# Kernel tuning notes

Hardware: AMD Instinct MI355X
Metric: run time of the kernel (lower is better)

Reference implementation:

```python
import math
import jax, jax.numpy as jnp
import numpy as np

L, H, D, DFF = 4, 8, 1024, 4096
RGB, AUD = 1024, 128
D_ATT, D_HOP, NCLS = 128, 4, 3862
B, T = 32, 300
EPS = 1e-6


def setup_inputs() -> dict:
    key = jax.random.key(0)
    ks = iter(jax.random.split(key, 40))
    s = 0.02
    p = {
        'padded_frame_rgbs': jax.random.uniform(next(ks), (B, T, RGB), jnp.float32),
        'padded_frame_audios': jax.random.uniform(next(ks), (B, T, AUD), jnp.float32),
        'embed_W': jax.random.normal(next(ks), (RGB + AUD, D), jnp.float32) * s,
        'embed_b': jnp.zeros((D,), jnp.float32),
        'Wq': jax.random.normal(next(ks), (L, D, D), jnp.float32) * s,
        'bq': jnp.zeros((L, D), jnp.float32),
        'Wk': jax.random.normal(next(ks), (L, D, D), jnp.float32) * s,
        'bk': jnp.zeros((L, D), jnp.float32),
        'Wv': jax.random.normal(next(ks), (L, D, D), jnp.float32) * s,
        'bv': jnp.zeros((L, D), jnp.float32),
        'Wo': jax.random.normal(next(ks), (L, D, D), jnp.float32) * s,
        'bo': jnp.zeros((L, D), jnp.float32),
        'ln1_a': jnp.ones((L, D), jnp.float32),
        'ln1_b': jnp.zeros((L, D), jnp.float32),
        'W1f': jax.random.normal(next(ks), (L, D, DFF), jnp.float32) * s,
        'b1f': jnp.zeros((L, DFF), jnp.float32),
        'W2f': jax.random.normal(next(ks), (L, DFF, D), jnp.float32) * s,
        'b2f': jnp.zeros((L, D), jnp.float32),
        'ln2_a': jnp.ones((L, D), jnp.float32),
        'ln2_b': jnp.zeros((L, D), jnp.float32),
        'fn_a': jnp.ones((D,), jnp.float32),
        'fn_b': jnp.zeros((D,), jnp.float32),
        'cw1': jax.random.normal(next(ks), (D, D_ATT), jnp.float32) * s,
        'cb1': jnp.zeros((D_ATT,), jnp.float32),
        'cw2': jax.random.normal(next(ks), (D_ATT, D_HOP), jnp.float32) * s,
        'cb2': jnp.zeros((D_HOP,), jnp.float32),
        'cw3': jax.random.normal(next(ks), (D_HOP * D, DFF), jnp.float32) * s,
        'cb3': jnp.zeros((DFF,), jnp.float32),
        'cw4': jax.random.normal(next(ks), (DFF, NCLS), jnp.float32) * s,
        'cb4': jnp.zeros((NCLS,), jnp.float32),
    }
    return p


def layernorm(x, a, b):
    # torch: a*(x-mean)/(std+eps)+b with unbiased std (ddof=1)
    mean = jnp.mean(x, axis=-1, keepdims=True)
    std = jnp.std(x, axis=-1, keepdims=True, ddof=1)
    return a * (x - mean) / (std + EPS) + b


def positional_encoding(T, D):
    pos = jnp.arange(T, dtype=jnp.float32)[:, None]
    div = jnp.exp(jnp.arange(0, D, 2, dtype=jnp.float32) * (-math.log(10000.0) / D))
    ang = pos * div  # [T, D/2]
    pe = jnp.stack([jnp.sin(ang), jnp.cos(ang)], axis=-1).reshape(T, D)
    return pe


def mha(x, Wq, bq, Wk, bk, Wv, bv, Wo, bo):
    dk = D // H
    q = (x @ Wq + bq).reshape(B, T, H, dk)
    k = (x @ Wk + bk).reshape(B, T, H, dk)
    v = (x @ Wv + bv).reshape(B, T, H, dk)
    scores = jnp.einsum('bthd,bshd->bhts', q, k) / math.sqrt(dk)
    p = jax.nn.softmax(scores, axis=-1)
    o = jnp.einsum('bhts,bshd->bthd', p, v).reshape(B, T, D)
    return o @ Wo + bo


def forward(padded_frame_rgbs, padded_frame_audios, embed_W, embed_b,
            Wq, bq, Wk, bk, Wv, bv, Wo, bo, ln1_a, ln1_b,
            W1f, b1f, W2f, b2f, ln2_a, ln2_b, fn_a, fn_b,
            cw1, cb1, cw2, cb2, cw3, cb3, cw4, cb4):
    feats = jnp.concatenate([padded_frame_rgbs / 255.0,
                             padded_frame_audios / 255.0], axis=2)
    x = (feats @ embed_W + embed_b) * math.sqrt(D)
    x = x + positional_encoding(T, D)[None]
    for i in range(L):
        x = x + mha(layernorm(x, ln1_a[i], ln1_b[i]),
                    Wq[i], bq[i], Wk[i], bk[i], Wv[i], bv[i], Wo[i], bo[i])
        h = layernorm(x, ln2_a[i], ln2_b[i])
        x = x + (jax.nn.relu(h @ W1f[i] + b1f[i]) @ W2f[i] + b2f[i])
    x = layernorm(x, fn_a, fn_b)
    # embedded classifier (multi-hop attention pooling)
    alpha = jnp.tanh(x @ cw1 + cb1) @ cw2 + cb2            # [B, T, D_HOP]
    alpha = jax.nn.softmax(alpha.transpose(0, 2, 1), -1)   # [B, D_HOP, T]
    ws = jnp.einsum('bht,btd->bhd', alpha, x).reshape(B, D_HOP * D)
    out = jnp.tanh(ws @ cw3 + cb3) @ cw4 + cb4             # [B, NCLS]
    return out, alpha


def reference(padded_frame_rgbs, padded_frame_audios, embed_W, embed_b,
              Wq, bq, Wk, bk, Wv, bv, Wo, bo, ln1_a, ln1_b,
              W1f, b1f, W2f, b2f, ln2_a, ln2_b, fn_a, fn_b,
              cw1, cb1, cw2, cb2, cw3, cb3, cw4, cb4):
    return forward(padded_frame_rgbs, padded_frame_audios, embed_W, embed_b,
                   Wq, bq, Wk, bk, Wv, bv, Wo, bo, ln1_a, ln1_b,
                   W1f, b1f, W2f, b2f, ln2_a, ln2_b, fn_a, fn_b,
                   cw1, cb1, cw2, cb2, cw3, cb3, cw4, cb4)
```

## Files before the change

### kernel.cpp

```cpp
#include <hip/hip_runtime.h>
#include <stdint.h>

#define NTOK 9600
#define TT   300
#define DD   1024
#define HH   8
#define DFF  4096
#define FIN  1152
#define DATT 128
#define NCLS 3862
#define TP   320
#define NQT  19

typedef unsigned short u16;
typedef __attribute__((ext_vector_type(8))) short short8;
typedef __attribute__((ext_vector_type(4))) float f32x4;

__device__ __forceinline__ int imin(int a, int b){ return a < b ? a : b; }

__device__ __forceinline__ u16 f2bf(float f){
    union { float f; uint32_t u; } v; v.f = f;
    uint32_t u = v.u;
    return (u16)((u + 0x7fffu + ((u >> 16) & 1u)) >> 16);
}
// ... 74 lines not shown
        const float* __restrict__ bk, const float* __restrict__ bv, float* __restrict__ out)
{
    const int i = blockIdx.x * 256 + threadIdx.x;
    if (i >= 4 * 3072) return;
    const int l = i / 3072, c = i % 3072;
    float v;
    if      (c < 1024) v = bq[l * 1024 + c];
    else if (c < 2048) v = bk[l * 1024 + c - 1024];
    else               v = bv[l * 1024 + c - 2048];
    out[i] = v;
}

template<int WF>
__global__ void __launch_bounds__(256) ln_kernel(const float* __restrict__ xin,
        const float* __restrict__ ga, const float* __restrict__ gb,
        u16* __restrict__ ob, float* of)
{
    const int row = blockIdx.x, t = threadIdx.x;
    const float4 xv = *(const float4*)(xin + (size_t)row * 1024 + t * 4);
    float s1 = xv.x + xv.y + xv.z + xv.w;
    float s2 = xv.x * xv.x + xv.y * xv.y + xv.z * xv.z + xv.w * xv.w;
    #pragma unroll
    for (int o = 1; o < 64; o <<= 1) { s1 += __shfl_xor(s1, o); s2 += __shfl_xor(s2, o); }
    __shared__ float r1[4], r2[4];
    const int lane = t & 63, wid = t >> 6;
    if (lane == 0) { r1[wid] = s1; r2[wid] = s2; }
    __syncthreads();
    s1 = r1[0] + r1[1] + r1[2] + r1[3];
    s2 = r2[0] + r2[1] + r2[2] + r2[3];
    const float mean = s1 * (1.0f / 1024.0f);
    const float var  = (s2 - 1024.0f * mean * mean) * (1.0f / 1023.0f);
    const float inv  = 1.0f / (sqrtf(fmaxf(var, 0.f)) + 1e-6f);
    const float4 av  = *(const float4*)(ga + t * 4);
    const float4 bv  = *(const float4*)(gb + t * 4);
    const float y0 = av.x * (xv.x - mean) * inv + bv.x;
    const float y1 = av.y * (xv.y - mean) * inv + bv.y;
    const float y2 = av.z * (xv.z - mean) * inv + bv.z;
    const float y3 = av.w * (xv.w - mean) * inv + bv.w;
    ushort4 o4; o4.x = f2bf(y0); o4.y = f2bf(y1); o4.z = f2bf(y2); o4.w = f2bf(y3);
    *(ushort4*)(ob + (size_t)row * 1024 + t * 4) = o4;
    if (WF) {
        float4 yo; yo.x = y0; yo.y = y1; yo.z = y2; yo.w = y3;
        *(float4*)(of + (size_t)row * 1024 + t * 4) = yo;
    }
}

#define EPI_EMBED        0
#define EPI_QKV          1
#define EPI_B_RELU_BF16  2
#define EPI_B_RES_F32    3
#define EPI_B_TANH_F32   4
#define EPI_ACC_F32      5
#define EPI_PART         6

template<int EPI, int SWZ>
__global__ void __launch_bounds__(256) gemm_k(const u16* __restrict__ A, const u16* __restrict__ Bt,
        const float* __restrict__ bias, const float* extra,
        float* outF, u16* outB, u16* outB2, u16* outB3, int M, int N, int K,
        int lda, int ldb, int kchunk)
{
    __shared__ __align__(16) u16 As[2][4096];
    __shared__ __align__(16) u16 Bs[2][4096];
    const int tid = threadIdx.x;
    int bm, bn;
    if (SWZ) {
        int lin = blockIdx.y * gridDim.x + blockIdx.x;
        const int nwg = gridDim.x * gridDim.y;
        const int cpx = nwg >> 3;
        lin = (lin & 7) * cpx + (lin >> 3);
        bm = lin / gridDim.x;
        bn = lin - bm * gridDim.x;
    } else {
        bm = blockIdx.y; bn = blockIdx.x;
    }
    const int lane = tid & 63, wid = tid >> 6;
    const int lg = lane >> 4, lr = lane & 15;
    const int wr = wid >> 1, wc = wid & 1;

    int koff = 0, Keff = K;
    if (kchunk > 0) { koff = blockIdx.z * kchunk; Keff = kchunk; }

    const int srow = tid >> 2;
    const int skc  = (tid & 3) * 8;
    const u16* ap0 = A  + (size_t)imin(bm * 128 + srow,      M - 1) * lda + skc + koff;
    const u16* ap1 = A  + (size_t)imin(bm * 128 + srow + 64, M - 1) * lda + skc + koff;
    const u16* bp0 = Bt + (size_t)imin(bn * 128 + srow,      N - 1) * ldb + skc + koff;
    const u16* bp1 = Bt + (size_t)imin(bn * 128 + srow + 64, N - 1) * ldb + skc + koff;

    f32x4 acc[4][4] = {};

    auto STAGE = [&](int b, int k0) {
        gll16(ap0 + k0, &As[b][tid * 8]);
        gll16(ap1 + k0, &As[b][2048 + tid * 8]);
        gll16(bp0 + k0, &Bs[b][tid * 8]);
        gll16(bp1 + k0, &Bs[b][2048 + tid * 8]);
    };
    auto COMPUTE = [&](int b) {
        short8 af[4], bf[4];
        #pragma unroll
        for (int m = 0; m < 4; ++m)
            af[m] = *(const short8*)(&As[b][(wr * 64 + m * 16 + lr) * 32 + lg * 8]);
        #pragma unroll
        for (int n = 0; n < 4; ++n)
            bf[n] = *(const short8*)(&Bs[b][(wc * 64 + n * 16 + lr) * 32 + lg * 8]);
        #pragma unroll
        for (int m = 0; m < 4; ++m)
            #pragma unroll
            for (int n = 0; n < 4; ++n)
                acc[m][n] = mfma16(af[m], bf[n], acc[m][n]);
    };

    STAGE(0, 0);
    __syncthreads();
    int cur = 0;
    for (int k0 = 32; k0 < Keff; k0 += 32) {
        STAGE(cur ^ 1, k0);
        COMPUTE(cur);
        __syncthreads();
        cur ^= 1;
    }
    COMPUTE(cur);

    #pragma unroll
    for (int m = 0; m < 4; ++m) {
        const int rb = bm * 128 + wr * 64 + m * 16 + lg * 4;
        #pragma unroll
        for (int n = 0; n < 4; ++n) {
            const int col = bn * 128 + wc * 64 + n * 16 + lr;
            if (col >= N) continue;
            const float bvl = (EPI == EPI_PART || EPI == EPI_ACC_F32) ? 0.f : bias[col];
            #pragma unroll
            for (int j = 0; j < 4; ++j) {
                const int r = rb + j;
                if (r >= M) continue;
                const float v = acc[m][n][j];
                const size_t oi = (size_t)r * N + col;
                if      (EPI == EPI_EMBED)       outF[oi] = (v + bvl) * 32.0f + extra[(size_t)(r % 300) * 1024 + col];
                else if (EPI == EPI_QKV) {
                    const int q = col >> 10, lc = col & 1023;
                    u16* dst = (q == 0) ? outB : ((q == 1) ? outB2 : outB3);
                    dst[(size_t)r * 1024 + lc] = f2bf(v + bvl);
                }
                else if (EPI == EPI_B_RELU_BF16) outB[oi] = f2bf(fmaxf(v + bvl, 0.f));
                else if (EPI == EPI_B_RES_F32)   outF[oi] = v + bvl + extra[oi];
                else if (EPI == EPI_B_TANH_F32)  outF[oi] = tanhf(v + bvl);
                else if (EPI == EPI_ACC_F32)     outF[oi] = v + extra[oi];
                else if (EPI == EPI_PART)        outF[(size_t)blockIdx.z * M * N + oi] = v;
            }
        }
    }
}

template<int EPI>
__global__ void __launch_bounds__(512, 2) gemm_big(const u16* __restrict__ A, const u16* __restrict__ Bt,
        const float* __restrict__ bias, const float* __restrict__ extra,
        float* outF, u16* outB, u16* outB2, u16* outB3,
        int M, int N, int K, int lda, int ldb, int kchunk)
{
    __shared__ __align__(16) u16 LA[2][256 * 32];
    __shared__ __align__(16) u16 LB[2][256 * 32];
    const int tid = threadIdx.x;
    int lin = blockIdx.x;
    const int nwg = gridDim.x;
    if ((nwg & 7) == 0) { const int cpx = nwg >> 3; lin = (lin & 7) * cpx + (lin >> 3); }
    int z = 0;
    if (kchunk > 0) { z = lin & 1; lin >>= 1; }
    const int ntN = N >> 8;
    const int bm = lin / ntN, bn = lin - (lin / ntN) * ntN;
    const int koff = z * kchunk;
    const int Keff = (kchunk > 0) ? kchunk : K;

    const int lane = tid & 63, wid = tid >> 6;
    const int wm = wid >> 2, wn = wid & 3;
    const int lg = lane >> 4, lr = lane & 15;

    const int prow = tid >> 2;
    const int skg  = (((tid & 3) ^ ((tid >> 3) & 3)) * 8);
    const u16* asrc0 = A  + (size_t)imin(bm * 256 + prow,       M - 1) * lda + skg + koff;
    const u16* asrc1 = A  + (size_t)imin(bm * 256 + prow + 128, M - 1) * lda + skg + koff;
    const u16* bsrc0 = Bt + (size_t)(bn * 256 + prow)       * ldb + skg + koff;
    const u16* bsrc1 = Bt + (size_t)(bn * 256 + prow + 128) * ldb + skg + koff;

    auto STAGE = [&](int s, int k0) {
        gll16(asrc0 + k0, &LA[s][tid * 8]);
        gll16(asrc1 + k0, &LA[s][4096 + tid * 8]);
        gll16(bsrc0 + k0, &LB[s][tid * 8]);
        gll16(bsrc1 + k0, &LB[s][4096 + tid * 8]);
    };

    const int kge = (lg ^ ((lr >> 1) & 3)) * 8;
    int aoff[8], boff[4];
    #pragma unroll
    for (int m = 0; m < 8; ++m) aoff[m] = (wm * 128 + m * 16 + lr) * 32 + kge;
    #pragma unroll
    for (int n = 0; n < 4; ++n) boff[n] = (wn * 64 + n * 16 + lr) * 32 + kge;

    f32x4 acc[8][4] = {};
    short8 af[8], bf[4];

    const int nk = Keff >> 5;
    STAGE(0, 0);
    STAGE(1, 32);
    asm volatile("s_waitcnt vmcnt(4)" ::: "memory");
    asm volatile("s_barrier" ::: "memory");
    __builtin_amdgcn_sched_barrier(0);

    auto BODY = [&](int t, int s, bool doStage) {
        #pragma unroll
        for (int m = 0; m < 8; ++m) af[m] = *(const short8*)(&LA[s][aoff[m]]);
        #pragma unroll
        for (int n = 0; n < 4; ++n) bf[n] = *(const short8*)(&LB[s][boff[n]]);
        asm volatile("s_waitcnt lgkmcnt(0)" ::: "memory");
        __builtin_amdgcn_sched_barrier(0);
        __builtin_amdgcn_s_setprio(1);
        #pragma unroll
        for (int m = 0; m < 4; ++m)
            #pragma unroll
            for (int n = 0; n < 4; ++n)
                acc[m][n] = mfma16(af[m], bf[n], acc[m][n]);
        __builtin_amdgcn_s_setprio(0);
        asm volatile("s_barrier" ::: "memory");
        __builtin_amdgcn_sched_barrier(0);
        if (doStage) STAGE(s, (t + 2) * 32);
        __builtin_amdgcn_s_setprio(1);
        #pragma unroll
        for (int m = 4; m < 8; ++m)
            #pragma unroll
            for (int n = 0; n < 4; ++n)
                acc[m][n] = mfma16(af[m], bf[n], acc[m][n]);
        __builtin_amdgcn_s_setprio(0);
    };

    for (int t = 0; t < nk - 2; ++t) {
        BODY(t, t & 1, true);
        asm volatile("s_waitcnt vmcnt(4)" ::: "memory");
        __builtin_amdgcn_sched_barrier(0);
        asm volatile("s_barrier" ::: "memory");
        __builtin_amdgcn_sched_barrier(0);
    }
    BODY(nk - 2, (nk - 2) & 1, false);
    asm volatile("s_waitcnt vmcnt(0)" ::: "memory");
    __builtin_amdgcn_sched_barrier(0);
    asm volatile("s_barrier" ::: "memory");
    __builtin_amdgcn_sched_barrier(0);
    BODY(nk - 1, (nk - 1) & 1, false);

    #pragma unroll
    for (int m = 0; m < 8; ++m) {
        const int rb = bm * 256 + wm * 128 + m * 16 + lg * 4;
        #pragma unroll
        for (int n = 0; n < 4; ++n) {
            const int col = bn * 256 + wn * 64 + n * 16 + lr;
            const float bvl = (EPI == EPI_PART) ? 0.f : bias[col];
            #pragma unroll
            for (int j = 0; j < 4; ++j) {
                const int r = rb + j;
                if (r >= M) continue;
                const float v = acc[m][n][j] + bvl;
                const size_t oi = (size_t)r * N + col;
                if (EPI == EPI_QKV) {
                    const int q = col >> 10, lc = col & 1023;
                    u16* dst = (q == 0) ? outB : ((q == 1) ? outB2 : outB3);
                    dst[(size_t)r * 1024 + lc] = f2bf(v);
                }
                else if (EPI == EPI_B_RELU_BF16) outB[oi] = f2bf(fmaxf(v, 0.f));
                else if (EPI == EPI_B_RES_F32)   outF[oi] = v + extra[oi];
                else if (EPI == EPI_EMBED)       outF[oi] = v * 32.0f + extra[(size_t)(r % 300) * 1024 + col];
                else if (EPI == EPI_PART)        outF[(size_t)z * M * N + oi] = v;
            }
        }
    }
}

template<int EPI>
__global__ void __launch_bounds__(256, 3) gemm_mid(const u16* __restrict__ A, const u16* __restrict__ Bt,
        const float* __restrict__ bias, const float* __restrict__ extra,
        float* outF, u16* outB, u16* outB2, u16* outB3,
        int M, int N, int K, int lda, int ldb)
{
    __shared__ __align__(16) u16 LA[2][128 * 32];
    __shared__ __align__(16) u16 LB[2][128 * 32];
    const int tid = threadIdx.x;
    int lin = blockIdx.x;
    const int nwg = gridDim.x;
    if ((nwg & 7) == 0) { const int cpx = nwg >> 3; lin = (lin & 7) * cpx + (lin >> 3); }
    const int ntN = N >> 7;
    const int bm = lin / ntN, bn = lin - (lin / ntN) * ntN;

    const int lane = tid & 63, wid = tid >> 6;
    const int wr = wid >> 1, wc = wid & 1;
    const int lg = lane >> 4, lr = lane & 15;

    const int prow = tid >> 2;
    const int skg  = (((tid & 3) ^ ((tid >> 3) & 3)) * 8);
    const u16* asrc0 = A  + (size_t)imin(bm * 128 + prow,      M - 1) * lda + skg;
    const u16* asrc1 = A  + (size_t)imin(bm * 128 + prow + 64, M - 1) * lda + skg;
    const u16* bsrc0 = Bt + (size_t)(bn * 128 + prow)      * ldb + skg;
    const u16* bsrc1 = Bt + (size_t)(bn * 128 + prow + 64) * ldb + skg;

    auto STAGE = [&](int s, int k0) {
        gll16(asrc0 + k0, &LA[s][tid * 8]);
        gll16(asrc1 + k0, &LA[s][2048 + tid * 8]);
        gll16(bsrc0 + k0, &LB[s][tid * 8]);
        gll16(bsrc1 + k0, &LB[s][2048 + tid * 8]);
    };

    const int kge = (lg ^ ((lr >> 1) & 3)) * 8;
    int aoff[4], boff[4];
    #pragma unroll
    for (int m = 0; m < 4; ++m) aoff[m] = (wr * 64 + m * 16 + lr) * 32 + kge;
    #pragma unroll
    for (int n = 0; n < 4; ++n) boff[n] = (wc * 64 + n * 16 + lr) * 32 + kge;

    f32x4 acc[4][4] = {};
    short8 af[4], bf[4];

    const int nk = K >> 5;
    STAGE(0, 0);
    STAGE(1, 32);
    asm volatile("s_waitcnt vmcnt(4)" ::: "memory");
    asm volatile("s_barrier" ::: "memory");
    __builtin_amdgcn_sched_barrier(0);

    auto BODY = [&](int t, int s, bool doStage) {
        #pragma unroll
        for (int m = 0; m < 4; ++m) af[m] = *(const short8*)(&LA[s][aoff[m]]);
        #pragma unroll
        for (int n = 0; n < 4; ++n) bf[n] = *(const short8*)(&LB[s][boff[n]]);
        __builtin_amdgcn_s_setprio(1);
        #pragma unroll
        for (int m = 0; m < 2; ++m)
            #pragma unroll
            for (int n = 0; n < 4; ++n)
                acc[m][n] = mfma16(af[m], bf[n], acc[m][n]);
        __builtin_amdgcn_s_setprio(0);
        asm volatile("s_waitcnt lgkmcnt(0)" ::: "memory");
        __builtin_amdgcn_sched_barrier(0);
        asm volatile("s_barrier" ::: "memory");
        __builtin_amdgcn_sched_barrier(0);
        if (doStage) STAGE(s, (t + 2) * 32);
        __builtin_amdgcn_s_setprio(1);
        #pragma unroll
        for (int m = 2; m < 4; ++m)
            #pragma unroll
            for (int n = 0; n < 4; ++n)
                acc[m][n] = mfma16(af[m], bf[n], acc[m][n]);
        __builtin_amdgcn_s_setprio(0);
    };

    for (int t = 0; t < nk - 2; ++t) {
        BODY(t, t & 1, true);
        asm volatile("s_waitcnt vmcnt(4)" ::: "memory");
        __builtin_amdgcn_sched_barrier(0);
        asm volatile("s_barrier" ::: "memory");
        __builtin_amdgcn_sched_barrier(0);
    }
    BODY(nk - 2, (nk - 2) & 1, false);
    asm volatile("s_waitcnt vmcnt(0)" ::: "memory");
    __builtin_amdgcn_sched_barrier(0);
    asm volatile("s_barrier" ::: "memory");
    __builtin_amdgcn_sched_barrier(0);
    BODY(nk - 1, (nk - 1) & 1, false);

    #pragma unroll
    for (int m = 0; m < 4; ++m) {
        const int rb = bm * 128 + wr * 64 + m * 16 + lg * 4;
        #pragma unroll
        for (int n = 0; n < 4; ++n) {
            const int col = bn * 128 + wc * 64 + n * 16 + lr;
            const float bvl = bias[col];
            #pragma unroll
            for (int j = 0; j < 4; ++j) {
                const int r = rb + j;
                if (r >= M) continue;
                const float v = acc[m][n][j] + bvl;
                const size_t oi = (size_t)r * N + col;
                if      (EPI == EPI_B_RES_F32)   outF[oi] = v + extra[oi];
                else if (EPI == EPI_EMBED)       outF[oi] = v * 32.0f + extra[(size_t)(r % 300) * 1024 + col];
                else if (EPI == EPI_B_RELU_BF16) outB[oi] = f2bf(fmaxf(v, 0.f));
                else if (EPI == EPI_B_TANH_F32)  outF[oi] = tanhf(v);
                else if (EPI == EPI_QKV) {
                    const int q = col >> 10, lc = col & 1023;
                    u16* dst = (q == 0) ? outB : ((q == 1) ? outB2 : outB3);
                    dst[(size_t)r * 1024 + lc] = f2bf(v);
                }
            }
        }
    }
}

template<int TANH>
__global__ void __launch_bounds__(256) redk_kernel(const float* __restrict__ part,
        const float* __restrict__ bias, float* outF, u16* outB, int M, int N, int Z)
{
    const int i = blockIdx.x * 256 + threadIdx.x;
    if (i >= M * N) return;
    const int col = i % N;
    float s = 0.f;
    for (int z = 0; z < Z; ++z) s += part[(size_t)z * M * N + i];
    s += bias[col];
    if (TANH) outB[i] = f2bf(tanhf(s));
    else      outF[i] = s;
}

__global__ void __launch_bounds__(512) attn_scores_kernel(const u16* __restrict__ Qb,
        const u16* __restrict__ Kb, u16* __restrict__ P)
{
    __shared__ __align__(16) u16 Ks[304 * 128];
    __shared__ __align__(16) u16 Ps[8][16][TP];
    const int bh = blockIdx.x, b = bh >> 3, h = bh & 7;
    const int tid = threadIdx.x, lane = tid & 63, wid = tid >> 6;
    const int lg = lane >> 4, lr = lane & 15;

    for (int c = tid; c < 304 * 16; c += 512) {
        const int kv = c >> 4, part = c & 15;
        const int tok = b * 300 + imin(kv, 299);
        const short8 v = *(const short8*)(Kb + (size_t)tok * 1024 + h * 128 + part * 8);
        int byte_ = kv * 256 + part * 16;
        byte_ ^= (kv & 7) << 4;
        *(short8*)((char*)Ks + byte_) = v;
    }
    __syncthreads();

    const float scale = 0.08838834764831845f;
    for (int qt = wid; qt < NQT; qt += 8) {
        f32x4 acc[NQT] = {};
        const int qtok = b * 300 + imin(qt * 16 + lr, 299);
        const u16* qrow = Qb + (size_t)qtok * 1024 + h * 128;
        #pragma unroll
        for (int kk = 0; kk < 4; ++kk) {
            const short8 aq = *(const short8*)(qrow + kk * 32 + lg * 8);
            #pragma unroll
            for (int nt = 0; nt < NQT; ++nt) {
                const int kvrow = nt * 16 + lr;
                int byte_ = kvrow * 256 + kk * 64 + lg * 16;
                byte_ ^= (kvrow & 7) << 4;
                const short8 bk = *(const short8*)((char*)Ks + byte_);
                acc[nt] = mfma16(aq, bk, acc[nt]);
            }
        }
        const int sw = lg << 3;
        #pragma unroll
        for (int j = 0; j < 4; ++j) {
            float vals[NQT];
            float m = -1e30f;
            #pragma unroll
            for (int nt = 0; nt < NQT; ++nt) {
                float s = acc[nt][j] * scale;
                if (nt * 16 + lr >= 300) s = -1e30f;
                vals[nt] = s;
                m = fmaxf(m, s);
            }
            #pragma unroll
            for (int o = 1; o < 16; o <<= 1) m = fmaxf(m, __shfl_xor(m, o));
            float sum = 0.f;
            #pragma unroll
            for (int nt = 0; nt < NQT; ++nt) { const float e = __expf(vals[nt] - m); vals[nt] = e; sum += e; }
            #pragma unroll
            for (int o = 1; o < 16; o <<= 1) sum += __shfl_xor(sum, o);
            const float inv = 1.0f / sum;
            const int row = lg * 4 + j;
            #pragma unroll
            for (int nt = 0; nt < NQT; ++nt) Ps[wid][row][(nt * 16 + lr) ^ sw] = f2bf(vals[nt] * inv);
            Ps[wid][row][(304 + lr) ^ sw] = 0;
        }
        asm volatile("s_waitcnt lgkmcnt(0)" ::: "memory");
        __builtin_amdgcn_sched_barrier(0);
        #pragma unroll
        for (int it = 0; it < 10; ++it) {
            const int idx = it * 64 + lane;
            const int row = idx / 40, c8 = idx - row * 40;
            const int swr = ((row >> 2) & 3) << 3;
            const short8 v8 = *(const short8*)(&Ps[wid][row][(c8 * 8) ^ swr]);
            const int q = qt * 16 + row;
            if (q < 300) *(short8*)(P + ((size_t)bh * 300 + q) * TP + c8 * 8) = v8;
        }
    }
}

__global__ void __launch_bounds__(512) attn_pv_kernel(const u16* __restrict__ P,
        const u16* __restrict__ Vb, u16* __restrict__ O)
{
    __shared__ __align__(16) u16 Vs[128 * TP];
    __shared__ __align__(16) u16 Os[8][16][128];
    const int bh = blockIdx.x, b = bh >> 3, h = bh & 7;
    const int tid = threadIdx.x, lane = tid & 63, wid = tid >> 6;
    const int lg = lane >> 4, lr = lane & 15;

    for (int c = tid; c < 304 * 16; c += 512) {
        const int kv = c >> 4, dp = c & 15;
        const int tok = b * 300 + imin(kv, 299);
        const short8 v = *(const short8*)(Vb + (size_t)tok * 1024 + h * 128 + dp * 8);
        #pragma unroll
        for (int jj = 0; jj < 8; ++jj) {
            const int d = dp * 8 + jj;
            int byte_ = d * (TP * 2) + kv * 2;
            byte_ ^= (d & 7) << 4;
            *(u16*)((char*)Vs + byte_) = (u16)v[jj];
        }
    }
    for (int c = tid; c < 128 * 16; c += 512) {
        const int d = c >> 4, kv = 304 + (c & 15);
        int byte_ = d * (TP * 2) + kv * 2;
        byte_ ^= (d & 7) << 4;
        *(u16*)((char*)Vs + byte_) = 0;
    }
    __syncthreads();

    for (int qt = wid; qt < NQT; qt += 8) {
        f32x4 acc[8] = {};
        const int q = imin(qt * 16 + lr, 299);
        const u16* prow = P + ((size_t)bh * 300 + q) * TP;
        #pragma unroll
        for (int kk = 0; kk < 10; ++kk) {
            const short8 ap = *(const short8*)(prow + kk * 32 + lg * 8);
            #pragma unroll
            for (int nt = 0; nt < 8; ++nt) {
                const int d = nt * 16 + lr;
                int byte_ = d * (TP * 2) + kk * 64 + lg * 16;
                byte_ ^= (d & 7) << 4;
                const short8 bv8 = *(const short8*)((char*)Vs + byte_);
                acc[nt] = mfma16(ap, bv8, acc[nt]);
            }
        }
        const int sw = lg << 3;
        #pragma unroll
        for (int nt = 0; nt < 8; ++nt)
            #pragma unroll
            for (int j = 0; j < 4; ++j)
                Os[wid][lg * 4 + j][(nt * 16 + lr) ^ sw] = f2bf(acc[nt][j]);
        asm volatile("s_waitcnt lgkmcnt(0)" ::: "memory");
        __builtin_amdgcn_sched_barrier(0);
        #pragma unroll
        for (int it = 0; it < 4; ++it) {
            const int idx = it * 64 + lane;
            const int row = idx >> 4, c8 = idx & 15;
            const int swr = ((row >> 2) & 3) << 3;
            const short8 v8 = *(const short8*)(&Os[wid][row][(c8 * 8) ^ swr]);
            const int qq = qt * 16 + row;
            if (qq < 300)
                *(short8*)(O + ((size_t)(b * 300 + qq)) * 1024 + h * 128 + c8 * 8) = v8;
        }
    }
}

__global__ void __launch_bounds__(256) logits_kernel(const float* __restrict__ a1,
        const float* __restrict__ cw2, const float* __restrict__ cb2, float* __restrict__ out)
{
    const int tok = blockIdx.x * 4 + (threadIdx.x >> 6);
    const int lane = threadIdx.x & 63;
    if (tok >= NTOK) return;
    const float v0 = a1[(size_t)tok * 128 + lane];
    const float v1 = a1[(size_t)tok * 128 + 64 + lane];
    #pragma unroll
    for (int hp = 0; hp < 4; ++hp) {
        float s = v0 * cw2[lane * 4 + hp] + v1 * cw2[(64 + lane) * 4 + hp];
        #pragma unroll
        for (int o = 1; o < 64; o <<= 1) s += __shfl_xor(s, o);
        if (lane == 0) out[(size_t)tok * 4 + hp] = s + cb2[hp];
    }
}

__global__ void __launch_bounds__(512) softmaxT_kernel(const float* __restrict__ lgt,
        float* __restrict__ alpha, float* __restrict__ outAlpha)
{
    const int bh = blockIdx.x;
    const int b = bh >> 2, hp = bh & 3;
    const int t = threadIdx.x;
    const float v = (t < 300) ? lgt[((size_t)(b * 300 + t)) * 4 + hp] : -1e30f;
    float m = v;
    #pragma unroll
    for (int o = 1; o < 64; o <<= 1) m = fmaxf(m, __shfl_xor(m, o));
    __shared__ float rm[8], rs[8];
    const int lane = t & 63, wid = t >> 6;
    if (lane == 0) rm[wid] = m;
    __syncthreads();
    m = rm[0];
    #pragma unroll
    for (int i = 1; i < 8; ++i) m = fmaxf(m, rm[i]);
    const float e = (t < 300) ? __expf(v - m) : 0.f;
    float s = e;
    #pragma unroll
    for (int o = 1; o < 64; o <<= 1) s += __shfl_xor(s, o);
    if (lane == 0) rs[wid] = s;
    __syncthreads();
    s = rs[0] + rs[1] + rs[2] + rs[3] + rs[4] + rs[5] + rs[6] + rs[7];
    if (t < 300) {
        const float a = e / s;
        alpha[(size_t)bh * 300 + t] = a;
        outAlpha[(size_t)bh * 300 + t] = a;
    }
}

__global__ void __launch_bounds__(256) pool_kernel(const float* __restrict__ alpha,
        const float* __restrict__ xln, float* __restrict__ wsp)
{
    const int bh = blockIdx.x, b = bh >> 2;
    const int d = blockIdx.y * 256 + threadIdx.x;
    const float* xp = xln + (size_t)b * 300 * 1024 + d;
    const float* al = alpha + (size_t)bh * 300;
    float acc = 0.f;
    for (int t = 0; t < 300; ++t) acc += al[t] * xp[(size_t)t * 1024];
    wsp[(size_t)bh * 1024 + d] = acc;
}

extern "C" void kernel_launch(void* const* d_in, const int* in_sizes, int n_in,
                              void* d_out, int out_size, void* d_ws, size_t ws_size,
                              hipStream_t stream)
{
    const float* rgb     = (const float*)d_in[0];
    const float* aud     = (const float*)d_in[1];
    const float* embed_W = (const float*)d_in[2];
    const float* embed_b = (const float*)d_in[3];
    const float* Wq      = (const float*)d_in[4];
    const float* bq      = (const float*)d_in[5];
    const float* Wk      = (const float*)d_in[6];
    const float* bk      = (const float*)d_in[7];
    const float* Wv      = (const float*)d_in[8];
    const float* bv      = (const float*)d_in[9];
    const float* Wo      = (const float*)d_in[10];
    const float* bo      = (const float*)d_in[11];
    const float* ln1_a   = (const float*)d_in[12];
    const float* ln1_b   = (const float*)d_in[13];
    const float* W1f     = (const float*)d_in[14];
    const float* b1f     = (const float*)d_in[15];
    const float* W2f     = (const float*)d_in[16];
    const float* b2f     = (const float*)d_in[17];
    const float* ln2_a   = (const float*)d_in[18];
    const float* ln2_b   = (const float*)d_in[19];
    const float* fn_a    = (const float*)d_in[20];
    const float* fn_b    = (const float*)d_in[21];
    const float* cw1     = (const float*)d_in[22];
    const float* cb1     = (const float*)d_in[23];
    const float* cw2     = (const float*)d_in[24];
    const float* cb2     = (const float*)d_in[25];
    const float* cw3     = (const float*)d_in[26];
    const float* cb3     = (const float*)d_in[27];
    const float* cw4     = (const float*)d_in[28];
    const float* cb4     = (const float*)d_in[29];

    const bool bigS = ws_size >= ((size_t)238 << 20);
    const size_t Ssz = bigS ? (size_t)NTOK * DFF * 2 : (size_t)256 * 300 * TP * 2;

    char* base = (char*)d_ws;
    size_t off = 0;
    auto alloc = [&](size_t bytes) -> char* {
        char* p = base + off; off += (bytes + 255) & ~(size_t)255; return p; };

    float* x    = (float*)alloc((size_t)NTOK * DD * 4);
    float* pe   = (float*)alloc((size_t)TT * DD * 4);
    u16*  hbuf  = (u16*) alloc((size_t)NTOK * DD * 2);
    u16*  Qb    = (u16*) alloc((size_t)NTOK * DD * 2);
    u16*  Kb    = (u16*) alloc((size_t)NTOK * DD * 2);
    u16*  Vb    = (u16*) alloc((size_t)NTOK * DD * 2);
    u16*  S     = (u16*) alloc(Ssz);
    float* lgts = (float*)alloc((size_t)NTOK * 4 * 4);
    float* alph = (float*)alloc((size_t)128 * 300 * 4);
    float* wsp  = (float*)alloc((size_t)32 * 4096 * 4);
    u16*  wsb   = (u16*) alloc((size_t)32 * 4096 * 2);
    u16*  t3b   = (u16*) alloc((size_t)32 * 4096 * 2);
    float* bqkv = (float*)alloc((size_t)4 * 3072 * 4);
    u16*  eWt   = (u16*) alloc((size_t)1024 * 1152 * 2);
    u16*  WqkvT = (u16*) alloc((size_t)3 * 1024 * 1024 * 2);
    u16*  WoT   = (u16*) alloc((size_t)1024 * 1024 * 2);
    u16*  W1T   = (u16*) alloc((size_t)DFF * DD * 2);
    u16*  W2T   = (u16*) alloc((size_t)DD * DFF * 2);
    u16*  c1T   = (u16*) alloc((size_t)128 * 1024 * 2);
    if (off > ws_size) return;

    u16*  featsb = S;
    u16*  pbuf   = S;
    u16*  midc   = S;
    u16*  Ob     = hbuf;
    float* xln   = (float*)Qb;
    u16*  xlnb   = Vb;
    float* a1    = (float*)S;
    u16*  c3T    = (u16*)x;
    u16*  c4T    = S;
    float* part  = (float*)hbuf;
    float* outv     = (float*)d_out;
    float* outAlpha = outv + (size_t)32 * NCLS;

    const dim3 blk(256);

    pe_kernel<<<(TT * DD + 255) / 256, blk, 0, stream>>>(pe);
    feats_kernel<<<(int)(((size_t)NTOK * FIN + 255) / 256), blk, 0, stream>>>(rgb, aud, featsb);
    qkvbias_kernel<<<(4 * 3072 + 255) / 256, blk, 0, stream>>>(bq, bk, bv, bqkv);

    auto wconv = [&](const float* W, u16* Wt, int K, int N) {
        dim3 g((N + 31) / 32, (K + 31) / 32);
        wconv_kernel<<<g, dim3(32, 8), 0, stream>>>(W, Wt, K, N);
    };
    wconv(embed_W, eWt, FIN, DD);
    wconv(cw1, c1T, DD, DATT);

    gemm_mid<EPI_EMBED><<<600, blk, 0, stream>>>(featsb, eWt, embed_b, pe, x,
            nullptr, nullptr, nullptr, NTOK, DD, FIN, FIN, FIN);

    for (int i = 0; i < 4; ++i) {
        wconv3_kernel<<<dim3(32, 32, 3), dim3(32, 8), 0, stream>>>(
                Wq + (size_t)i * DD * DD, Wk + (size_t)i * DD * DD, Wv + (size_t)i * DD * DD, WqkvT);
        wconv(Wo  + (size_t)i * DD * DD,  WoT, DD, DD);
        wconv(W1f + (size_t)i * DD * DFF, W1T, DD, DFF);
        wconv(W2f + (size_t)i * DFF * DD, W2T, DFF, DD);

        ln_kernel<0><<<NTOK, blk, 0, stream>>>(x, ln1_a + (size_t)i * DD, ln1_b + (size_t)i * DD, hbuf, nullptr);
        gemm_mid<EPI_QKV><<<1800, blk, 0, stream>>>(hbuf, WqkvT, bqkv + (size_t)i * 3072, nullptr,
                nullptr, Qb, Kb, Vb, NTOK, 3072, DD, DD, DD);
        attn_scores_kernel<<<256, dim3(512), 0, stream>>>(Qb, Kb, pbuf);
        attn_pv_kernel<<<256, dim3(512), 0, stream>>>(pbuf, Vb, Ob);
        gemm_mid<EPI_B_RES_F32><<<600, blk, 0, stream>>>(Ob, WoT, bo + (size_t)i * DD, x, x,
                nullptr, nullptr, nullptr, NTOK, DD, DD, DD, DD);
        ln_kernel<0><<<NTOK, blk, 0, stream>>>(x, ln2_a + (size_t)i * DD, ln2_b + (size_t)i * DD, hbuf, nullptr);
        if (bigS) {
            gemm_mid<EPI_B_RELU_BF16><<<2400, blk, 0, stream>>>(hbuf, W1T, b1f + (size_t)i * DFF,
                    nullptr, nullptr, midc, nullptr, nullptr, NTOK, DFF, DD, DD, DD);
            gemm_mid<EPI_B_RES_F32><<<600, blk, 0, stream>>>(midc, W2T, b2f + (size_t)i * DD, x, x,
                    nullptr, nullptr, nullptr, NTOK, DD, DFF, DFF, DFF);
        } else {
            for (int h = 0; h < 2; ++h) {
                gemm_big<EPI_B_RELU_BF16><<<304, dim3(512), 0, stream>>>(hbuf, W1T + (size_t)h * 2048 * DD,
                        b1f + (size_t)i * DFF + h * 2048, nullptr, nullptr, midc, nullptr, nullptr,
                        NTOK, 2048, DD, DD, DD, 0);
                if (h == 0)
                    gemm_k<EPI_B_RES_F32, 1><<<dim3(8, 75), blk, 0, stream>>>(midc, W2T + (size_t)h * 2048,
                            b2f + (size_t)i * DD, x, x, nullptr, nullptr, nullptr, NTOK, DD, 2048, 2048, DFF, 0);
                else
                    gemm_k<EPI_ACC_F32, 1><<<dim3(8, 75), blk, 0, stream>>>(midc, W2T + (size_t)h * 2048,
                            b2f + (size_t)i * DD, x, x, nullptr, nullptr, nullptr, NTOK, DD, 2048, 2048, DFF, 0);
            }
        }
    }

    ln_kernel<1><<<NTOK, blk, 0, stream>>>(x, fn_a, fn_b, xlnb, xln);
    wconv(cw3, c3T, 4096, DFF);
    gemm_mid<EPI_B_TANH_F32><<<75, blk, 0, stream>>>(xlnb, c1T, cb1, nullptr, a1,
            nullptr, nullptr, nullptr, NTOK, DATT, DD, DD, DD);
    logits_kernel<<<2400, blk, 0, stream>>>(a1, cw2, cb2, lgts);
    wconv(cw4, c4T, DFF, NCLS);
    softmaxT_kernel<<<128, dim3(512), 0, stream>>>(lgts, alph, outAlpha);
    pool_kernel<<<dim3(128, 4), blk, 0, stream>>>(alph, xln, wsp);
    f2bf_kernel<<<(32 * 4096 + 255) / 256, blk, 0, stream>>>(wsp, wsb, 32 * 4096);

    gemm_k<EPI_PART, 0><<<dim3(32, 1, 8), blk, 0, stream>>>(wsb, c3T, nullptr, nullptr, part,
            nullptr, nullptr, nullptr, 32, 4096, 4096, 4096, 4096, 512);
    redk_kernel<1><<<(32 * 4096 + 255) / 256, blk, 0, stream>>>(part, cb3, nullptr, t3b, 32, 4096, 8);
    gemm_k<EPI_PART, 0><<<dim3(31, 1, 8), blk, 0, stream>>>(t3b, c4T, nullptr, nullptr, part,
            nullptr, nullptr, nullptr, 32, NCLS, 4096, 4096, 4096, 512);
    redk_kernel<0><<<(32 * NCLS + 255) / 256, blk, 0, stream>>>(part, cb4, outv, nullptr, 32, NCLS, 8);
}
```

Before: 2.079 ms.

## Split attention kernels across two blocks per head to double grid size

The attention score kernel now launches two blocks per (batch, head), each handling half of the query tiles, and writes softmax probabilities directly to global memory instead of staging through shared memory. The PV kernel splits the 128-wide head dimension into two 64-wide halves per block, halving its shared V tile and output staging. Both get launch_bounds occupancy hints and a 512-block grid to fill more compute units than the previous 256 blocks. The costs are that the score kernel reloads the full K tile in each half-block, and its direct stores are scattered 2-byte writes rather than coalesced 16-byte ones. With 10 query tiles per half and 8 waves, some waves also do two iterations while others idle.

Measured after the change: 2.808 ms. 35.0% more time.

```diff
diff --git a/kernel.cpp b/kernel.cpp
--- a/kernel.cpp
+++ b/kernel.cpp
@@ -501,12 +501,12 @@
     else      outF[i] = s;
 }
 
-__global__ void __launch_bounds__(512) attn_scores_kernel(const u16* __restrict__ Qb,
+__global__ void __launch_bounds__(512, 4) attn_scores_kernel(const u16* __restrict__ Qb,
         const u16* __restrict__ Kb, u16* __restrict__ P)
 {
     __shared__ __align__(16) u16 Ks[304 * 128];
-    __shared__ __align__(16) u16 Ps[8][16][TP];
-    const int bh = blockIdx.x, b = bh >> 3, h = bh & 7;
+    const int bh = blockIdx.x >> 1, half = blockIdx.x & 1;
+    const int b = bh >> 3, h = bh & 7;
     const int tid = threadIdx.x, lane = tid & 63, wid = tid >> 6;
     const int lg = lane >> 4, lr = lane & 15;
 
@@ -521,7 +521,8 @@
     __syncthreads();
 
     const float scale = 0.08838834764831845f;
-    for (int qt = wid; qt < NQT; qt += 8) {
+    const int qtEnd = imin(NQT, half * 10 + 10);
+    for (int qt = half * 10 + wid; qt < qtEnd; qt += 8) {
         f32x4 acc[NQT] = {};
         const int qtok = b * 300 + imin(qt * 16 + lr, 299);
         const u16* qrow = Qb + (size_t)qtok * 1024 + h * 128;
@@ -537,7 +538,6 @@
                 acc[nt] = mfma16(aq, bk, acc[nt]);
             }
         }
-        const int sw = lg << 3;
         #pragma unroll
         for (int j = 0; j < 4; ++j) {
             float vals[NQT];
@@ -557,38 +557,31 @@
             #pragma unroll
             for (int o = 1; o < 16; o <<= 1) sum += __shfl_xor(sum, o);
             const float inv = 1.0f / sum;
-            const int row = lg * 4 + j;
-            #pragma unroll
-            for (int nt = 0; nt < NQT; ++nt) Ps[wid][row][(nt * 16 + lr) ^ sw] = f2bf(vals[nt] * inv);
-            Ps[wid][row][(304 + lr) ^ sw] = 0;
+            const int q = qt * 16 + lg * 4 + j;
+            if (q < 300) {
+                u16* prow = P + ((size_t)bh * 300 + q) * TP;
+                #pragma unroll
+                for (int nt = 0; nt < NQT; ++nt) prow[nt * 16 + lr] = f2bf(vals[nt] * inv);
+                prow[304 + lr] = 0;
+            }
         }
-        asm volatile("s_waitcnt lgkmcnt(0)" ::: "memory");
-        __builtin_amdgcn_sched_barrier(0);
-        #pragma unroll
-        for (int it = 0; it < 10; ++it) {
-            const int idx = it * 64 + lane;
-            const int row = idx / 40, c8 = idx - row * 40;
-            const int swr = ((row >> 2) & 3) << 3;
-            const short8 v8 = *(const short8*)(&Ps[wid][row][(c8 * 8) ^ swr]);
-            const int q = qt * 16 + row;
-            if (q < 300) *(short8*)(P + ((size_t)bh * 300 + q) * TP + c8 * 8) = v8;
-        }
-    }
-}
-
-__global__ void __launch_bounds__(512) attn_pv_kernel(const u16* __restrict__ P,
+    }
+}
+
+__global__ void __launch_bounds__(512, 4) attn_pv_kernel(const u16* __restrict__ P,
         const u16* __restrict__ Vb, u16* __restrict__ O)
 {
-    __shared__ __align__(16) u16 Vs[128 * TP];
-    __shared__ __align__(16) u16 Os[8][16][128];
-    const int bh = blockIdx.x, b = bh >> 3, h = bh & 7;
+    __shared__ __align__(16) u16 Vs[64 * TP];
+    __shared__ __align__(16) u16 Os[8][16][64];
+    const int bh = blockIdx.x >> 1, dh = blockIdx.x & 1;
+    const int b = bh >> 3, h = bh & 7;
     const int tid = threadIdx.x, lane = tid & 63, wid = tid >> 6;
     const int lg = lane >> 4, lr = lane & 15;
 
-    for (int c = tid; c < 304 * 16; c += 512) {
-        const int kv = c >> 4, dp = c & 15;
+    for (int c = tid; c < 304 * 8; c += 512) {
+        const int kv = c >> 3, dp = c & 7;
         const int tok = b * 300 + imin(kv, 299);
-        const short8 v = *(const short8*)(Vb + (size_t)tok * 1024 + h * 128 + dp * 8);
+        const short8 v = *(const short8*)(Vb + (size_t)tok * 1024 + h * 128 + dh * 64 + dp * 8);
         #pragma unroll
         for (int jj = 0; jj < 8; ++jj) {
             const int d = dp * 8 + jj;
@@ -597,7 +590,7 @@
             *(u16*)((char*)Vs + byte_) = (u16)v[jj];
         }
     }
-    for (int c = tid; c < 128 * 16; c += 512) {
+    for (int c = tid; c < 64 * 16; c += 512) {
         const int d = c >> 4, kv = 304 + (c & 15);
         int byte_ = d * (TP * 2) + kv * 2;
         byte_ ^= (d & 7) << 4;
@@ -606,14 +599,14 @@
     __syncthreads();
 
     for (int qt = wid; qt < NQT; qt += 8) {
-        f32x4 acc[8] = {};
+        f32x4 acc[4] = {};
         const int q = imin(qt * 16 + lr, 299);
         const u16* prow = P + ((size_t)bh * 300 + q) * TP;
         #pragma unroll
         for (int kk = 0; kk < 10; ++kk) {
             const short8 ap = *(const short8*)(prow + kk * 32 + lg * 8);
             #pragma unroll
-            for (int nt = 0; nt < 8; ++nt) {
+            for (int nt = 0; nt < 4; ++nt) {
                 const int d = nt * 16 + lr;
                 int byte_ = d * (TP * 2) + kk * 64 + lg * 16;
                 byte_ ^= (d & 7) << 4;
@@ -623,21 +616,21 @@
         }
         const int sw = lg << 3;
         #pragma unroll
-        for (int nt = 0; nt < 8; ++nt)
+        for (int nt = 0; nt < 4; ++nt)
             #pragma unroll
             for (int j = 0; j < 4; ++j)
                 Os[wid][lg * 4 + j][(nt * 16 + lr) ^ sw] = f2bf(acc[nt][j]);
         asm volatile("s_waitcnt lgkmcnt(0)" ::: "memory");
         __builtin_amdgcn_sched_barrier(0);
         #pragma unroll
-        for (int it = 0; it < 4; ++it) {
+        for (int it = 0; it < 2; ++it) {
             const int idx = it * 64 + lane;
-            const int row = idx >> 4, c8 = idx & 15;
+            const int row = idx >> 3, c8 = idx & 7;
             const int swr = ((row >> 2) & 3) << 3;
             const short8 v8 = *(const short8*)(&Os[wid][row][(c8 * 8) ^ swr]);
             const int qq = qt * 16 + row;
             if (qq < 300)
-                *(short8*)(O + ((size_t)(b * 300 + qq)) * 1024 + h * 128 + c8 * 8) = v8;
+                *(short8*)(O + ((size_t)(b * 300 + qq)) * 1024 + h * 128 + dh * 64 + c8 * 8) = v8;
         }
     }
 }
@@ -805,8 +798,8 @@
         ln_kernel<0><<<NTOK, blk, 0, stream>>>(x, ln1_a + (size_t)i * DD, ln1_b + (size_t)i * DD, hbuf, nullptr);
         gemm_mid<EPI_QKV><<<1800, blk, 0, stream>>>(hbuf, WqkvT, bqkv + (size_t)i * 3072, nullptr,
                 nullptr, Qb, Kb, Vb, NTOK, 3072, DD, DD, DD);
-        attn_scores_kernel<<<256, dim3(512), 0, stream>>>(Qb, Kb, pbuf);
-        attn_pv_kernel<<<256, dim3(512), 0, stream>>>(pbuf, Vb, Ob);
+        attn_scores_kernel<<<512, dim3(512), 0, stream>>>(Qb, Kb, pbuf);
+        attn_pv_kernel<<<512, dim3(512), 0, stream>>>(pbuf, Vb, Ob);
         gemm_mid<EPI_B_RES_F32><<<600, blk, 0, stream>>>(Ob, WoT, bo + (size_t)i * DD, x, x,
                 nullptr, nullptr, nullptr, NTOK, DD, DD, DD, DD);
         ln_kernel<0><<<NTOK, blk, 0, stream>>>(x, ln2_a + (size_t)i * DD, ln2_b + (size_t)i * DD, hbuf, nullptr);
```

## Add 128x128 GEMM with 64-wide K step and use it for most projections

Applied to the files above, without the earlier changes.

Adds gemm_mid64, a 128x128-tile GEMM that stages 64 K-elements per iteration with a wider XOR swizzle and splits the MFMA work into two halves so the second half's LDS reads overlap the first half's compute. It replaces gemm_mid for the embed, QKV, output projection and FFN paths, and replaces the 256x256 gemm_big for the FFN up-projection. The aim is to halve barrier and loop overhead per K and improve latency hiding. In exchange each block uses twice the LDS with occupancy lowered to 2, and the FFN1 path loses the larger tile's data reuse.

After: 2.308 ms. 11.0% more time.

```diff
diff --git a/kernel.cpp b/kernel.cpp
--- a/kernel.cpp
+++ b/kernel.cpp
@@ -250,127 +250,6 @@
 }
 
 template<int EPI>
-__global__ void __launch_bounds__(512, 2) gemm_big(const u16* __restrict__ A, const u16* __restrict__ Bt,
-        const float* __restrict__ bias, const float* __restrict__ extra,
-        float* outF, u16* outB, u16* outB2, u16* outB3,
-        int M, int N, int K, int lda, int ldb, int kchunk)
-{
-    __shared__ __align__(16) u16 LA[2][256 * 32];
-    __shared__ __align__(16) u16 LB[2][256 * 32];
-    const int tid = threadIdx.x;
-    int lin = blockIdx.x;
-    const int nwg = gridDim.x;
-    if ((nwg & 7) == 0) { const int cpx = nwg >> 3; lin = (lin & 7) * cpx + (lin >> 3); }
-    int z = 0;
-    if (kchunk > 0) { z = lin & 1; lin >>= 1; }
-    const int ntN = N >> 8;
-    const int bm = lin / ntN, bn = lin - (lin / ntN) * ntN;
-    const int koff = z * kchunk;
-    const int Keff = (kchunk > 0) ? kchunk : K;
-
-    const int lane = tid & 63, wid = tid >> 6;
-    const int wm = wid >> 2, wn = wid & 3;
-    const int lg = lane >> 4, lr = lane & 15;
-
-    const int prow = tid >> 2;
-    const int skg  = (((tid & 3) ^ ((tid >> 3) & 3)) * 8);
-    const u16* asrc0 = A  + (size_t)imin(bm * 256 + prow,       M - 1) * lda + skg + koff;
-    const u16* asrc1 = A  + (size_t)imin(bm * 256 + prow + 128, M - 1) * lda + skg + koff;
-    const u16* bsrc0 = Bt + (size_t)(bn * 256 + prow)       * ldb + skg + koff;
-    const u16* bsrc1 = Bt + (size_t)(bn * 256 + prow + 128) * ldb + skg + koff;
-
-    auto STAGE = [&](int s, int k0) {
-        gll16(asrc0 + k0, &LA[s][tid * 8]);
-        gll16(asrc1 + k0, &LA[s][4096 + tid * 8]);
-        gll16(bsrc0 + k0, &LB[s][tid * 8]);
-        gll16(bsrc1 + k0, &LB[s][4096 + tid * 8]);
-    };
-
-    const int kge = (lg ^ ((lr >> 1) & 3)) * 8;
-    int aoff[8], boff[4];
-    #pragma unroll
-    for (int m = 0; m < 8; ++m) aoff[m] = (wm * 128 + m * 16 + lr) * 32 + kge;
-    #pragma unroll
-    for (int n = 0; n < 4; ++n) boff[n] = (wn * 64 + n * 16 + lr) * 32 + kge;
-
-    f32x4 acc[8][4] = {};
-    short8 af[8], bf[4];
-
-    const int nk = Keff >> 5;
-    STAGE(0, 0);
-    STAGE(1, 32);
-    asm volatile("s_waitcnt vmcnt(4)" ::: "memory");
-    asm volatile("s_barrier" ::: "memory");
-    __builtin_amdgcn_sched_barrier(0);
-
-    auto BODY = [&](int t, int s, bool doStage) {
-        #pragma unroll
-        for (int m = 0; m < 8; ++m) af[m] = *(const short8*)(&LA[s][aoff[m]]);
-        #pragma unroll
-        for (int n = 0; n < 4; ++n) bf[n] = *(const short8*)(&LB[s][boff[n]]);
-        asm volatile("s_waitcnt lgkmcnt(0)" ::: "memory");
-        __builtin_amdgcn_sched_barrier(0);
-        __builtin_amdgcn_s_setprio(1);
-        #pragma unroll
-        for (int m = 0; m < 4; ++m)
-            #pragma unroll
-            for (int n = 0; n < 4; ++n)
-                acc[m][n] = mfma16(af[m], bf[n], acc[m][n]);
-        __builtin_amdgcn_s_setprio(0);
-        asm volatile("s_barrier" ::: "memory");
-        __builtin_amdgcn_sched_barrier(0);
-        if (doStage) STAGE(s, (t + 2) * 32);
-        __builtin_amdgcn_s_setprio(1);
-        #pragma unroll
-        for (int m = 4; m < 8; ++m)
-            #pragma unroll
-            for (int n = 0; n < 4; ++n)
-                acc[m][n] = mfma16(af[m], bf[n], acc[m][n]);
-        __builtin_amdgcn_s_setprio(0);
-    };
-
-    for (int t = 0; t < nk - 2; ++t) {
-        BODY(t, t & 1, true);
-        asm volatile("s_waitcnt vmcnt(4)" ::: "memory");
-        __builtin_amdgcn_sched_barrier(0);
-        asm volatile("s_barrier" ::: "memory");
-        __builtin_amdgcn_sched_barrier(0);
-    }
-    BODY(nk - 2, (nk - 2) & 1, false);
-    asm volatile("s_waitcnt vmcnt(0)" ::: "memory");
-    __builtin_amdgcn_sched_barrier(0);
-    asm volatile("s_barrier" ::: "memory");
-    __builtin_amdgcn_sched_barrier(0);
-    BODY(nk - 1, (nk - 1) & 1, false);
-
-    #pragma unroll
-    for (int m = 0; m < 8; ++m) {
-        const int rb = bm * 256 + wm * 128 + m * 16 + lg * 4;
-        #pragma unroll
-        for (int n = 0; n < 4; ++n) {
-            const int col = bn * 256 + wn * 64 + n * 16 + lr;
-            const float bvl = (EPI == EPI_PART) ? 0.f : bias[col];
-            #pragma unroll
-            for (int j = 0; j < 4; ++j) {
-                const int r = rb + j;
-                if (r >= M) continue;
-                const float v = acc[m][n][j] + bvl;
-                const size_t oi = (size_t)r * N + col;
-                if (EPI == EPI_QKV) {
-                    const int q = col >> 10, lc = col & 1023;
-                    u16* dst = (q == 0) ? outB : ((q == 1) ? outB2 : outB3);
-                    dst[(size_t)r * 1024 + lc] = f2bf(v);
-                }
-                else if (EPI == EPI_B_RELU_BF16) outB[oi] = f2bf(fmaxf(v, 0.f));
-                else if (EPI == EPI_B_RES_F32)   outF[oi] = v + extra[oi];
-                else if (EPI == EPI_EMBED)       outF[oi] = v * 32.0f + extra[(size_t)(r % 300) * 1024 + col];
-                else if (EPI == EPI_PART)        outF[(size_t)z * M * N + oi] = v;
-            }
-        }
-    }
-}
-
-template<int EPI>
 __global__ void __launch_bounds__(256, 3) gemm_mid(const u16* __restrict__ A, const u16* __restrict__ Bt,
         const float* __restrict__ bias, const float* __restrict__ extra,
         float* outF, u16* outB, u16* outB2, u16* outB3,
@@ -477,6 +356,133 @@
                 else if (EPI == EPI_EMBED)       outF[oi] = v * 32.0f + extra[(size_t)(r % 300) * 1024 + col];
                 else if (EPI == EPI_B_RELU_BF16) outB[oi] = f2bf(fmaxf(v, 0.f));
                 else if (EPI == EPI_B_TANH_F32)  outF[oi] = tanhf(v);
+                else if (EPI == EPI_QKV) {
+                    const int q = col >> 10, lc = col & 1023;
+                    u16* dst = (q == 0) ? outB : ((q == 1) ? outB2 : outB3);
+                    dst[(size_t)r * 1024 + lc] = f2bf(v);
+                }
+            }
+        }
+    }
+}
+
+template<int EPI>
+__global__ void __launch_bounds__(256, 2) gemm_mid64(const u16* __restrict__ A, const u16* __restrict__ Bt,
+        const float* __restrict__ bias, const float* __restrict__ extra,
+        float* outF, u16* outB, u16* outB2, u16* outB3,
+        int M, int N, int K, int lda, int ldb)
+{
+    __shared__ __align__(16) u16 LA[2][128 * 64];
+    __shared__ __align__(16) u16 LB[2][128 * 64];
+    const int tid = threadIdx.x;
+    int lin = blockIdx.x;
+    const int nwg = gridDim.x;
+    if ((nwg & 7) == 0) { const int cpx = nwg >> 3; lin = (lin & 7) * cpx + (lin >> 3); }
+    const int ntN = N >> 7;
+    const int bm = lin / ntN, bn = lin - (lin / ntN) * ntN;
+
+    const int lane = tid & 63, wid = tid >> 6;
+    const int wr = wid >> 1, wc = wid & 1;
+    const int lg = lane >> 4, lr = lane & 15;
+
+    const int prow = tid >> 3;
+    const int skg  = (((tid & 7) ^ ((tid >> 3) & 7)) * 8);
+    const u16* asrc[4];
+    const u16* bsrc[4];
+    #pragma unroll
+    for (int L = 0; L < 4; ++L) {
+        asrc[L] = A  + (size_t)imin(bm * 128 + L * 32 + prow, M - 1) * lda + skg;
+        bsrc[L] = Bt + (size_t)(bn * 128 + L * 32 + prow) * ldb + skg;
+    }
+
+    auto STAGE = [&](int s, int k0) {
+        #pragma unroll
+        for (int L = 0; L < 4; ++L) gll16(asrc[L] + k0, &LA[s][L * 2048 + tid * 8]);
+        #pragma unroll
+        for (int L = 0; L < 4; ++L) gll16(bsrc[L] + k0, &LB[s][L * 2048 + tid * 8]);
+    };
+
+    int aoff[2][4], boff[2][4];
+    #pragma unroll
+    for (int c = 0; c < 2; ++c) {
+        #pragma unroll
+        for (int m = 0; m < 4; ++m)
+            aoff[c][m] = (wr * 64 + m * 16 + lr) * 64 + ((((c << 2) + lg) ^ (lr & 7)) * 8);
+        #pragma unroll
+        for (int n = 0; n < 4; ++n)
+            boff[c][n] = (wc * 64 + n * 16 + lr) * 64 + ((((c << 2) + lg) ^ (lr & 7)) * 8);
+    }
+
+    f32x4 acc[4][4] = {};
+    short8 af0[4], bf0[4], af1[4], bf1[4];
+
+    const int nk = K >> 6;
+    STAGE(0, 0);
+    STAGE(1, 64);
+    asm volatile("s_waitcnt vmcnt(8)" ::: "memory");
+    asm volatile("s_barrier" ::: "memory");
+    __builtin_amdgcn_sched_barrier(0);
+
+    auto BODY = [&](int t, int s, bool doStage) {
+        #pragma unroll
+        for (int m = 0; m < 4; ++m) af0[m] = *(const short8*)(&LA[s][aoff[0][m]]);
+        #pragma unroll
+        for (int n = 0; n < 4; ++n) bf0[n] = *(const short8*)(&LB[s][boff[0][n]]);
+        __builtin_amdgcn_s_setprio(1);
+        #pragma unroll
+        for (int m = 0; m < 4; ++m)
+            #pragma unroll
+            for (int n = 0; n < 4; ++n)
+                acc[m][n] = mfma16(af0[m], bf0[n], acc[m][n]);
+        __builtin_amdgcn_s_setprio(0);
+        #pragma unroll
+        for (int m = 0; m < 4; ++m) af1[m] = *(const short8*)(&LA[s][aoff[1][m]]);
+        #pragma unroll
+        for (int n = 0; n < 4; ++n) bf1[n] = *(const short8*)(&LB[s][boff[1][n]]);
+        asm volatile("s_waitcnt lgkmcnt(0)" ::: "memory");
+        __builtin_amdgcn_sched_barrier(0);
+        asm volatile("s_barrier" ::: "memory");
+        __builtin_amdgcn_sched_barrier(0);
+        if (doStage) STAGE(s, (t + 2) * 64);
+        __builtin_amdgcn_s_setprio(1);
+        #pragma unroll
+        for (int m = 0; m < 4; ++m)
+            #pragma unroll
+            for (int n = 0; n < 4; ++n)
+                acc[m][n] = mfma16(af1[m], bf1[n], acc[m][n]);
+        __builtin_amdgcn_s_setprio(0);
+    };
+
+    for (int t = 0; t < nk - 2; ++t) {
+        BODY(t, t & 1, true);
+        asm volatile("s_waitcnt vmcnt(8)" ::: "memory");
+        __builtin_amdgcn_sched_barrier(0);
+        asm volatile("s_barrier" ::: "memory");
+        __builtin_amdgcn_sched_barrier(0);
+    }
+    BODY(nk - 2, (nk - 2) & 1, false);
+    asm volatile("s_waitcnt vmcnt(0)" ::: "memory");
+    __builtin_amdgcn_sched_barrier(0);
+    asm volatile("s_barrier" ::: "memory");
+    __builtin_amdgcn_sched_barrier(0);
+    BODY(nk - 1, (nk - 1) & 1, false);
+
+    #pragma unroll
+    for (int m = 0; m < 4; ++m) {
+        const int rb = bm * 128 + wr * 64 + m * 16 + lg * 4;
+        #pragma unroll
+        for (int n = 0; n < 4; ++n) {
+            const int col = bn * 128 + wc * 64 + n * 16 + lr;
+            const float bvl = bias[col];
+            #pragma unroll
+            for (int j = 0; j < 4; ++j) {
+                const int r = rb + j;
+                if (r >= M) continue;
+                const float v = acc[m][n][j] + bvl;
+                const size_t oi = (size_t)r * N + col;
+                if      (EPI == EPI_B_RES_F32)   outF[oi] = v + extra[oi];
+                else if (EPI == EPI_EMBED)       outF[oi] = v * 32.0f + extra[(size_t)(r % 300) * 1024 + col];
+                else if (EPI == EPI_B_RELU_BF16) outB[oi] = f2bf(fmaxf(v, 0.f));
                 else if (EPI == EPI_QKV) {
                     const int q = col >> 10, lc = col & 1023;
                     u16* dst = (q == 0) ? outB : ((q == 1) ? outB2 : outB3);
@@ -792,7 +798,7 @@
     wconv(embed_W, eWt, FIN, DD);
     wconv(cw1, c1T, DD, DATT);
 
-    gemm_mid<EPI_EMBED><<<600, blk, 0, stream>>>(featsb, eWt, embed_b, pe, x,
+    gemm_mid64<EPI_EMBED><<<600, blk, 0, stream>>>(featsb, eWt, embed_b, pe, x,
             nullptr, nullptr, nullptr, NTOK, DD, FIN, FIN, FIN);
 
     for (int i = 0; i < 4; ++i) {
@@ -803,23 +809,23 @@
         wconv(W2f + (size_t)i * DFF * DD, W2T, DFF, DD);
 
         ln_kernel<0><<<NTOK, blk, 0, stream>>>(x, ln1_a + (size_t)i * DD, ln1_b + (size_t)i * DD, hbuf, nullptr);
-        gemm_mid<EPI_QKV><<<1800, blk, 0, stream>>>(hbuf, WqkvT, bqkv + (size_t)i * 3072, nullptr,
+        gemm_mid64<EPI_QKV><<<1800, blk, 0, stream>>>(hbuf, WqkvT, bqkv + (size_t)i * 3072, nullptr,
                 nullptr, Qb, Kb, Vb, NTOK, 3072, DD, DD, DD);
         attn_scores_kernel<<<256, dim3(512), 0, stream>>>(Qb, Kb, pbuf);
         attn_pv_kernel<<<256, dim3(512), 0, stream>>>(pbuf, Vb, Ob);
-        gemm_mid<EPI_B_RES_F32><<<600, blk, 0, stream>>>(Ob, WoT, bo + (size_t)i * DD, x, x,
+        gemm_mid64<EPI_B_RES_F32><<<600, blk, 0, stream>>>(Ob, WoT, bo + (size_t)i * DD, x, x,
                 nullptr, nullptr, nullptr, NTOK, DD, DD, DD, DD);
         ln_kernel<0><<<NTOK, blk, 0, stream>>>(x, ln2_a + (size_t)i * DD, ln2_b + (size_t)i * DD, hbuf, nullptr);
         if (bigS) {
-            gemm_mid<EPI_B_RELU_BF16><<<2400, blk, 0, stream>>>(hbuf, W1T, b1f + (size_t)i * DFF,
+            gemm_mid64<EPI_B_RELU_BF16><<<2400, blk, 0, stream>>>(hbuf, W1T, b1f + (size_t)i * DFF,
                     nullptr, nullptr, midc, nullptr, nullptr, NTOK, DFF, DD, DD, DD);
-            gemm_mid<EPI_B_RES_F32><<<600, blk, 0, stream>>>(midc, W2T, b2f + (size_t)i * DD, x, x,
+            gemm_mid64<EPI_B_RES_F32><<<600, blk, 0, stream>>>(midc, W2T, b2f + (size_t)i * DD, x, x,
                     nullptr, nullptr, nullptr, NTOK, DD, DFF, DFF, DFF);
         } else {
             for (int h = 0; h < 2; ++h) {
-                gemm_big<EPI_B_RELU_BF16><<<304, dim3(512), 0, stream>>>(hbuf, W1T + (size_t)h * 2048 * DD,
+                gemm_mid64<EPI_B_RELU_BF16><<<1200, blk, 0, stream>>>(hbuf, W1T + (size_t)h * 2048 * DD,
                         b1f + (size_t)i * DFF + h * 2048, nullptr, nullptr, midc, nullptr, nullptr,
-                        NTOK, 2048, DD, DD, DD, 0);
+                        NTOK, 2048, DD, DD, DD);
                 if (h == 0)
                     gemm_k<EPI_B_RES_F32, 1><<<dim3(8, 75), blk, 0, stream>>>(midc, W2T + (size_t)h * 2048,
                             b2f + (size_t)i * DD, x, x, nullptr, nullptr, nullptr, NTOK, DD, 2048, 2048, DFF, 0);
```
